# Performance work log

Measured on AMD Instinct MI355X. Metric: run time of the kernel, lower is better.

The kernel has to match this reference:

```python
import jax, jax.numpy as jnp
import numpy as np

HEADS = 16
DIM_HEAD = 64
SCALE = DIM_HEAD ** -0.5


def setup_inputs() -> dict:
    key = jax.random.key(0)
    k1, k2, k3 = jax.random.split(key, 3)
    dim, inner = 1024, HEADS * DIM_HEAD
    b, n = 2, 2048
    x = jax.random.normal(k1, (b, n, dim), dtype=jnp.float32)
    w_qkv = jax.random.normal(k2, (dim, 3 * inner), dtype=jnp.float32) * (dim ** -0.5)
    w_out = jax.random.normal(k3, (inner, dim), dtype=jnp.float32) * (inner ** -0.5)
    b_out = jnp.zeros((dim,), dtype=jnp.float32)
    return {"x": x, "w_qkv": w_qkv, "w_out": w_out, "b_out": b_out}


def reference(x, w_qkv, w_out, b_out):
    b, n, _ = x.shape
    qkv = x @ w_qkv                                   # [b,n,3*inner]
    q, k, v = jnp.split(qkv, 3, axis=-1)
    def to_heads(t):
        return t.reshape(b, n, HEADS, DIM_HEAD).transpose(0, 2, 1, 3)  # [b,h,n,d]
    q, k, v = to_heads(q), to_heads(k), to_heads(v)
    dots = jnp.einsum('bhid,bhjd->bhij', q, k) * SCALE  # [b,h,n,n]
    attn = jax.nn.softmax(dots, axis=-1)
    out = jnp.einsum('bhij,bhjd->bhid', attn, v)        # [b,h,n,d]
    out = out.transpose(0, 2, 1, 3).reshape(b, n, HEADS * DIM_HEAD)
    return out @ w_out + b_out
```

## Files before the change

### kernel.cpp

```cpp
#include <hip/hip_runtime.h>
#include <hip/hip_bf16.h>

typedef unsigned short u16;
typedef unsigned int u32;
typedef __attribute__((ext_vector_type(8))) short short8;
typedef __attribute__((ext_vector_type(4))) float f32x4;
typedef __attribute__((ext_vector_type(16))) float f32x16;
typedef __attribute__((ext_vector_type(2))) u32 u32x2;

typedef __attribute__((address_space(1))) void as1_void;
typedef __attribute__((address_space(3))) void as3_void;

__device__ __forceinline__ u16 f2b(float x) {
    union { float f; u32 u; } c; c.f = x;
    u32 r = c.u + 0x7fffu + ((c.u >> 16) & 1u);
    return (u16)(r >> 16);
}
__device__ __forceinline__ float b2f(u16 x) {
    union { u32 u; float f; } c; c.u = ((u32)x) << 16;
    return c.f;
}
__device__ __forceinline__ u32 cvtpk(float lo, float hi) {
    u32 r;
    asm("v_cvt_pk_bf16_f32 %0, %1, %2" : "=v"(r) : "v"(lo), "v"(hi));
    return r;
}
__device__ __forceinline__ void gload16(const u16* g, u16* l) {
    __builtin_amdgcn_global_load_lds((as1_void*)(u16*)g, (as3_void*)l, 16, 0, 0);
}
__device__ __forceinline__ void barrier_raw() {
    asm volatile("" ::: "memory");
    __builtin_amdgcn_s_barrier();
    asm volatile("" ::: "memory");
}

__device__ __forceinline__ void tbody(const float* __restrict__ in, u16* __restrict__ out,
                                      int R, int C, int r0, int c0, int t,
                                      u16 (&tile)[64][72]) {
    {
        const int rr = t >> 2;
        const int cq = (t & 3) * 16;
        const float* src = in + (size_t)(r0 + rr) * C + c0 + cq;
        #pragma unroll
        for (int j = 0; j < 4; j++) {
            float4 v = *(const float4*)(src + j * 4);
            tile[cq + j*4 + 0][rr] = f2b(v.x);
            tile[cq + j*4 + 1][rr] = f2b(v.y);
            tile[cq + j*4 + 2][rr] = f2b(v.z);
            tile[cq + j*4 + 3][rr] = f2b(v.w);
        }
    }
    __syncthreads();
    {
        const int cc = t >> 2;
        const int rq = (t & 3) * 16;
        u16* dst = out + (size_t)(c0 + cc) * R + r0 + rq;
        *(short8*)(dst)     = *(const short8*)&tile[cc][rq];
        *(short8*)(dst + 8) = *(const short8*)&tile[cc][rq + 8];
    }
}

__global__ __launch_bounds__(256) void prep_fused(const float* __restrict__ x,
                                                  const float* __restrict__ w_qkv,
                                                  const float* __restrict__ w_out,
                                                  u16* __restrict__ xb,
                                                  u16* __restrict__ wqkvT,
                                                  u16* __restrict__ woutT) {
    __shared__ u16 tile[64][72];
    const int b = blockIdx.x, t = threadIdx.x;
    if (b < 2048) {
        const int i = b * 256 + t;
        const float4* p = (const float4*)(x + (size_t)i * 8);
        float4 a = p[0], c = p[1];
        short8 v;
        v[0]=(short)f2b(a.x); v[1]=(short)f2b(a.y); v[2]=(short)f2b(a.z); v[3]=(short)f2b(a.w);
        v[4]=(short)f2b(c.x); v[5]=(short)f2b(c.y); v[6]=(short)f2b(c.z); v[7]=(short)f2b(c.w);
        *(short8*)(xb + (size_t)i * 8) = v;
    } else if (b < 2816) {
        const int bb = b - 2048;
        tbody(w_qkv, wqkvT, 1024, 3072, (bb / 48) * 64, (bb % 48) * 64, t, tile);
    } else {
        const int bb = b - 2816;
        tbody(w_out, woutT, 1024, 1024, (bb >> 4) * 64, (bb & 15) * 64, t, tile);
    }
}

__global__ __launch_bounds__(256) void gemm128(const u16* __restrict__ A,
                                               const u16* __restrict__ Bt,
                                               u16* __restrict__ Cp,
                                               u16* __restrict__ vt,
                                               int M, int Nn, int K) {
    __shared__ __align__(16) u16 a_lds[2][128 * 32];
    __shared__ __align__(16) u16 b_lds[2][128 * 32];
    const int tid = threadIdx.x;
    const int w = tid >> 6, l = tid & 63;
    const int l16 = l & 15, lg = l >> 4;
    const int nbx = gridDim.x;
    const int flat = blockIdx.x + nbx * blockIdx.y;
    const int cpx = (nbx * gridDim.y) >> 3;
    const int logical = (flat & 7) * cpx + (flat >> 3);
    const int m0 = (logical / nbx) * 128, n0 = (logical % nbx) * 128;
    const int wm = w >> 1, wn = w & 1;
    const int lr = l >> 2;
    const int scol = (((l & 3) ^ ((lr >> 1) & 3)) * 8);
    const int rsl = (lg ^ ((l16 >> 1) & 3)) * 8;

    f32x4 acc[4][4];
    #pragma unroll
    for (int i = 0; i < 4; i++)
        #pragma unroll
        for (int j = 0; j < 4; j++) { f32x4 z = {0.f,0.f,0.f,0.f}; acc[i][j] = z; }

    const u16* Ap = A  + (size_t)m0 * K;
    const u16* Bp = Bt + (size_t)n0 * K;

#define STAGE(BUF, KOF)                                                              \
    _Pragma("unroll")                                                                \
    for (int j = 0; j < 2; j++) {                                                    \
        const int r = w * 32 + j * 16;                                               \
        gload16(Ap + (size_t)(r + lr) * K + (KOF) + scol, &a_lds[(BUF)][r * 32]);    \
        gload16(Bp + (size_t)(r + lr) * K + (KOF) + scol, &b_lds[(BUF)][r * 32]);    \
    }

    const int nk = K >> 5;
    STAGE(0, 0)
    int cur = 0;
    for (int kt = 0; kt < nk; kt++) {
        if (kt + 1 < nk) {
            STAGE(cur ^ 1, (kt + 1) << 5)
            __builtin_amdgcn_sched_barrier(0);
            asm volatile("s_waitcnt vmcnt(4)" ::: "memory");
            __builtin_amdgcn_sched_barrier(0);
        } else {
            __builtin_amdgcn_sched_barrier(0);
            asm volatile("s_waitcnt vmcnt(0)" ::: "memory");
            __builtin_amdgcn_sched_barrier(0);
        }
        barrier_raw();
        short8 af[4], bf8[4];
        #pragma unroll
        for (int mb = 0; mb < 4; mb++)
            af[mb] = *(const short8*)&a_lds[cur][(wm * 64 + mb * 16 + l16) * 32 + rsl];
        #pragma unroll
        for (int nb = 0; nb < 4; nb++)
            bf8[nb] = *(const short8*)&b_lds[cur][(wn * 64 + nb * 16 + l16) * 32 + rsl];
        #pragma unroll
        for (int mb = 0; mb < 4; mb++)
            #pragma unroll
            for (int nb = 0; nb < 4; nb++)
                acc[mb][nb] = __builtin_amdgcn_mfma_f32_16x16x32_bf16(af[mb], bf8[nb], acc[mb][nb], 0, 0, 0);
        barrier_raw();
        cur ^= 1;
    }
#undef STAGE

    #pragma unroll
    for (int mb = 0; mb < 4; mb++) {
        #pragma unroll
        for (int nb = 0; nb < 4; nb++) {
            const int col = n0 + wn * 64 + nb * 16 + l16;
            const int row0 = m0 + wm * 64 + mb * 16 + lg * 4;
            if (col < 2048) {
                #pragma unroll
                for (int r = 0; r < 4; r++)
                    Cp[(size_t)(row0 + r) * Nn + col] = f2b(acc[mb][nb][r]);
            } else {
                const int hd = col - 2048;
                const int hh = hd >> 6, d = hd & 63;
                const int bi = row0 >> 11, n = row0 & 2047;
                u32x2 pr;
                pr.x = cvtpk(acc[mb][nb][0], acc[mb][nb][1]);
                pr.y = cvtpk(acc[mb][nb][2], acc[mb][nb][3]);
                *(u32x2*)(vt + ((size_t)((bi * 16 + hh) * 64 + d)) * 2048 + n) = pr;
            }
        }
    }
}

__global__ __launch_bounds__(256) void gemm64n(const u16* __restrict__ A,
                                               const u16* __restrict__ Bt,
                                               float* __restrict__ Cp,
                                               const float* __restrict__ bias,
                                               int M, int Nn, int K) {
    __shared__ __align__(16) u16 a_lds[2][64 * 32];
    __shared__ __align__(16) u16 b_lds[2][128 * 32];
    const int tid = threadIdx.x;
    const int w = tid >> 6, l = tid & 63;
    const int l16 = l & 15, lg = l >> 4;
    const int nbx = gridDim.x;
    const int flat = blockIdx.x + nbx * blockIdx.y;
    const int cpx = (nbx * gridDim.y) >> 3;
    const int logical = (flat & 7) * cpx + (flat >> 3);
    const int m0 = (logical / nbx) * 64, n0 = (logical % nbx) * 128;
    const int wm = w >> 1, wn = w & 1;
    const int lr = l >> 2;
    const int scol = (((l & 3) ^ ((lr >> 1) & 3)) * 8);
    const int rsl = (lg ^ ((l16 >> 1) & 3)) * 8;

    f32x4 acc[2][4];
    #pragma unroll
    for (int i = 0; i < 2; i++)
        #pragma unroll
        for (int j = 0; j < 4; j++) { f32x4 z = {0.f,0.f,0.f,0.f}; acc[i][j] = z; }

    const u16* Ap = A  + (size_t)m0 * K;
    const u16* Bp = Bt + (size_t)n0 * K;

#define STAGE64(BUF, KOF)                                                            \
    gload16(Ap + (size_t)(w * 16 + lr) * K + (KOF) + scol, &a_lds[(BUF)][w * 16 * 32]); \
    _Pragma("unroll")                                                                \
    for (int j = 0; j < 2; j++) {                                                    \
        const int r = w * 32 + j * 16;                                               \
        gload16(Bp + (size_t)(r + lr) * K + (KOF) + scol, &b_lds[(BUF)][r * 32]);    \
    }

    const int nk = K >> 5;
    STAGE64(0, 0)
    int cur = 0;
    for (int kt = 0; kt < nk; kt++) {
        if (kt + 1 < nk) {
            STAGE64(cur ^ 1, (kt + 1) << 5)
            __builtin_amdgcn_sched_barrier(0);
            asm volatile("s_waitcnt vmcnt(3)" ::: "memory");
            __builtin_amdgcn_sched_barrier(0);
        } else {
            __builtin_amdgcn_sched_barrier(0);
            asm volatile("s_waitcnt vmcnt(0)" ::: "memory");
            __builtin_amdgcn_sched_barrier(0);
        }
        barrier_raw();
        short8 af[2], bf8[4];
        #pragma unroll
        for (int mb = 0; mb < 2; mb++)
            af[mb] = *(const short8*)&a_lds[cur][(wm * 32 + mb * 16 + l16) * 32 + rsl];
        #pragma unroll
        for (int nb = 0; nb < 4; nb++)
            bf8[nb] = *(const short8*)&b_lds[cur][(wn * 64 + nb * 16 + l16) * 32 + rsl];
        #pragma unroll
        for (int mb = 0; mb < 2; mb++)
            #pragma unroll
            for (int nb = 0; nb < 4; nb++)
                acc[mb][nb] = __builtin_amdgcn_mfma_f32_16x16x32_bf16(af[mb], bf8[nb], acc[mb][nb], 0, 0, 0);
        barrier_raw();
        cur ^= 1;
    }
#undef STAGE64

    #pragma unroll
    for (int mb = 0; mb < 2; mb++) {
        #pragma unroll
        for (int nb = 0; nb < 4; nb++) {
            const int col = n0 + wn * 64 + nb * 16 + l16;
            const int row0 = m0 + wm * 32 + mb * 16 + lg * 4;
            #pragma unroll
            for (int r = 0; r < 4; r++)
                Cp[(size_t)(row0 + r) * Nn + col] = acc[mb][nb][r] + bias[col];
        }
    }
}

__global__ __launch_bounds__(256, 2) void attn_kernel(const u16* __restrict__ qkv,
                                                      const u16* __restrict__ vt,
                                                      u16* __restrict__ out) {
    __shared__ __align__(16) u16 k_lds[16384];
    __shared__ __align__(16) u16 v_lds[16384];
    const int tid = threadIdx.x;
    const int w = tid >> 6, l = tid & 63;
    const int l31 = l & 31, hi = l >> 5;
    const int flat = blockIdx.x + (blockIdx.y << 4) + (blockIdx.z << 8);
    const int logical = (flat & 7) * 64 + (flat >> 3);
    const int xq = logical & 15, h = (logical >> 4) & 15, bb = logical >> 8;
    const int q0 = xq * 128 + w * 32;
    const int swzl = (l31 & 7) << 3;

    const u16* qp = qkv + (size_t)(bb * 2048 + q0 + l31) * 3072 + h * 64 + hi * 8;
    short8 qf[4];
    #pragma unroll
    for (int c4 = 0; c4 < 4; c4++) {
        short8 v = *(const short8*)(qp + c4 * 16);
        #pragma unroll
        for (int e = 0; e < 8; e++) v[e] = (short)f2b(b2f((u16)v[e]) * 0.125f);
        qf[c4] = v;
    }

    f32x16 o[2];
    #pragma unroll
    for (int d0 = 0; d0 < 2; d0++)
        #pragma unroll
        for (int e = 0; e < 16; e++) o[d0][e] = 0.f;
    float mrow = -1e30f, lsum = 0.f;

    const int srow = tid >> 2, sc = tid & 3;
    const int kd0 = srow * 64 + ((sc ^ (srow & 7)) * 8);
    const int kd1 = srow * 64 + (((sc + 4) ^ (srow & 7)) * 8);
    const u16* ksrc = qkv + (size_t)(bb * 2048 + srow) * 3072 + 1024 + h * 64 + sc * 8;
    const u16* vsrc = vt + (size_t)((bb * 16 + h) * 64 + srow) * 2048 + sc * 8;

    short8 kr0, kr1, vr0, vr1;
    kr0 = *(const short8*)ksrc; kr1 = *(const short8*)(ksrc + 32);
    vr0 = *(const short8*)vsrc; vr1 = *(const short8*)(vsrc + 32);
    ksrc += 64 * 3072; vsrc += 64;
    *(short8*)&k_lds[kd0] = kr0; *(short8*)&k_lds[kd1] = kr1;
    *(short8*)&v_lds[kd0] = vr0; *(short8*)&v_lds[kd1] = vr1;
    kr0 = *(const short8*)ksrc; kr1 = *(const short8*)(ksrc + 32);
    vr0 = *(const short8*)vsrc; vr1 = *(const short8*)(vsrc + 32);
    ksrc += 64 * 3072; vsrc += 64;
    *(short8*)&k_lds[4096 + kd0] = kr0; *(short8*)&k_lds[4096 + kd1] = kr1;
    *(short8*)&v_lds[4096 + kd0] = vr0; *(short8*)&v_lds[4096 + kd1] = vr1;
    __syncthreads();

#define DO_TILE(CUR, NXT)                                                               \
  {                                                                                     \
    kr0 = *(const short8*)ksrc; kr1 = *(const short8*)(ksrc + 32);                      \
    vr0 = *(const short8*)vsrc; vr1 = *(const short8*)(vsrc + 32);                      \
    ksrc += 64 * 3072; vsrc += 64;                                                      \
    f32x16 st[2];                                                                       \
    _Pragma("unroll") for (int tt = 0; tt < 2; tt++)                                    \
      _Pragma("unroll") for (int e = 0; e < 16; e++) st[tt][e] = 0.f;                   \
    _Pragma("unroll")                                                                   \
    for (int c4 = 0; c4 < 4; c4++) {                                                    \
      short8 kf0 = *(const short8*)&k_lds[(CUR) + (l31)*64      + ((c4*16 + hi*8) ^ swzl)]; \
      short8 kf1 = *(const short8*)&k_lds[(CUR) + (32 + l31)*64 + ((c4*16 + hi*8) ^ swzl)]; \
      st[0] = __builtin_amdgcn_mfma_f32_32x32x16_bf16(kf0, qf[c4], st[0], 0, 0, 0);     \
      st[1] = __builtin_amdgcn_mfma_f32_32x32x16_bf16(kf1, qf[c4], st[1], 0, 0, 0);     \
    }                                                                                   \
    float pmax = st[0][0];                                                              \
    _Pragma("unroll") for (int e = 1; e < 16; e++) pmax = fmaxf(pmax, st[0][e]);        \
    _Pragma("unroll") for (int e = 0; e < 16; e++) pmax = fmaxf(pmax, st[1][e]);        \
    const float rowm = fmaxf(pmax, __shfl_xor(pmax, 32));                               \
    if (__any(rowm > mrow + 5.5451774f)) {              \
      const float mnew  = fmaxf(mrow, rowm);                                            \
      const float alpha = __expf(mrow - mnew);                                          \
      lsum *= alpha;                                                                    \
      _Pragma("unroll") for (int d0 = 0; d0 < 2; d0++)                                  \
        _Pragma("unroll") for (int e = 0; e < 16; e++) o[d0][e] *= alpha;               \
      mrow = mnew;                                                                      \
    }                                                                                   \
    _Pragma("unroll") for (int tt = 0; tt < 2; tt++)                                    \
      _Pragma("unroll") for (int e = 0; e < 16; e++) st[tt][e] = __expf(st[tt][e] - mrow); \
    float psum = 0.f;                                                                   \
    _Pragma("unroll") for (int tt = 0; tt < 2; tt++)                                    \
      _Pragma("unroll") for (int e = 0; e < 16; e++) psum += st[tt][e];                 \
    lsum += psum + __shfl_xor(psum, 32);                                                \
    short8 pb[4];                                                                       \
    _Pragma("unroll")                                                                   \
    for (int tt = 0; tt < 2; tt++) {                                                    \
      _Pragma("unroll")                                                                 \
      for (int g = 0; g < 2; g++) {                                                     \
         \
        u32 w0 = cvtpk(st[tt][8*g + 0], st[tt][8*g + 1]);                               \
        u32 w1 = cvtpk(st[tt][8*g + 2], st[tt][8*g + 3]);                               \
        u32 w2 = cvtpk(st[tt][8*g + 4], st[tt][8*g + 5]);                               \
        u32 w3 = cvtpk(st[tt][8*g + 6], st[tt][8*g + 7]);                               \
        u32 w0x = (u32)__shfl_xor((int)w0, 32);                                         \
        u32 w1x = (u32)__shfl_xor((int)w1, 32);                                         \
        u32 w2x = (u32)__shfl_xor((int)w2, 32);                                         \
        u32 w3x = (u32)__shfl_xor((int)w3, 32);                                         \
        union { u32 wd[4]; short8 s8; } uu;                                             \
        uu.wd[0] = hi ? w2x : w0;                                                       \
        uu.wd[1] = hi ? w3x : w1;                                                       \
        uu.wd[2] = hi ? w2  : w0x;                                                      \
        uu.wd[3] = hi ? w3  : w1x;                                                      \
        pb[2*tt + g] = uu.s8;                                                           \
      }                                                                                 \
    }                                                                                   \
    _Pragma("unroll")                                                                   \
    for (int ks = 0; ks < 4; ks++) {                                                    \
      short8 vf0 = *(const short8*)&v_lds[(CUR) + (l31)*64      + ((ks*16 + hi*8) ^ swzl)]; \
      short8 vf1 = *(const short8*)&v_lds[(CUR) + (32 + l31)*64 + ((ks*16 + hi*8) ^ swzl)]; \
      o[0] = __builtin_amdgcn_mfma_f32_32x32x16_bf16(vf0, pb[ks], o[0], 0, 0, 0);       \
      o[1] = __builtin_amdgcn_mfma_f32_32x32x16_bf16(vf1, pb[ks], o[1], 0, 0, 0);       \
    }                                                                                   \
    *(short8*)&k_lds[(NXT) + kd0] = kr0; *(short8*)&k_lds[(NXT) + kd1] = kr1;           \
    *(short8*)&v_lds[(NXT) + kd0] = vr0; *(short8*)&v_lds[(NXT) + kd1] = vr1;           \
  }

    for (int it = 0; it < 8; it++) {
        DO_TILE(0, 8192)
        DO_TILE(4096, 12288)
        __syncthreads();
        DO_TILE(8192, 0)
        DO_TILE(12288, 4096)
        __syncthreads();
    }
#undef DO_TILE

    const float invl = 1.0f / lsum;
    u16* op = out + (size_t)(bb * 2048 + q0 + l31) * 1024 + h * 64;
    #pragma unroll
    for (int d0 = 0; d0 < 2; d0++) {
        #pragma unroll
        for (int s = 0; s < 4; s++) {
            u32x2 pr;
            pr.x = cvtpk(o[d0][4*s + 0] * invl, o[d0][4*s + 1] * invl);
            pr.y = cvtpk(o[d0][4*s + 2] * invl, o[d0][4*s + 3] * invl);
            *(u32x2*)(op + d0 * 32 + s * 8 + hi * 4) = pr;
        }
    }
}

extern "C" void kernel_launch(void* const* d_in, const int* in_sizes, int n_in,
                              void* d_out, int out_size, void* d_ws, size_t ws_size,
                              hipStream_t stream) {
    const float* x     = (const float*)d_in[0];
    const float* w_qkv = (const float*)d_in[1];
    const float* w_out = (const float*)d_in[2];
    const float* b_out = (const float*)d_in[3];

    char* ws = (char*)d_ws;
    u16* xb    = (u16*)(ws);
    u16* wqkvT = (u16*)(ws + (size_t)( 8u << 20));
    u16* woutT = (u16*)(ws + (size_t)(14u << 20));
    u16* qkvb  = (u16*)(ws + (size_t)(16u << 20));
    u16* vtb   = (u16*)(ws + (size_t)(40u << 20));
    u16* aout  = (u16*)(ws + (size_t)(48u << 20));

    prep_fused<<<3072, 256, 0, stream>>>(x, w_qkv, w_out, xb, wqkvT, woutT);

    gemm128<<<dim3(24, 32), 256, 0, stream>>>(xb, wqkvT, qkvb, vtb, 4096, 3072, 1024);
    attn_kernel<<<dim3(16, 16, 2), 256, 0, stream>>>(qkvb, vtb, aout);

    gemm64n<<<dim3(8, 64), 256, 0, stream>>>(aout, woutT, (float*)d_out, b_out,
                                             4096, 1024, 1024);
}
```

Baseline: 118.5 us.

## Stage attention K/V tiles directly into LDS using pre-swizzled global layouts

The QKV GEMM epilogue now writes K and the transposed V in an XOR-swizzled order inside each 64-element block. The attention kernel can then copy tiles straight from global memory into LDS with gload16, instead of loading into registers and storing with a swizzle. This is meant to cut VGPR pressure and VALU/LDS-store instructions in the main loop and to let loads for the next pair of tiles run while the current pair is computed. The prefetch in the last loop iteration fetches tiles past the sequence end, which may read out of bounds unless the load is bounds-checked.

```diff
diff --git a/kernel.cpp b/kernel.cpp
--- a/kernel.cpp
+++ b/kernel.cpp
@@ -160,18 +160,28 @@
         for (int nb = 0; nb < 4; nb++) {
             const int col = n0 + wn * 64 + nb * 16 + l16;
             const int row0 = m0 + wm * 64 + mb * 16 + lg * 4;
-            if (col < 2048) {
+            if (col < 1024) {
                 #pragma unroll
                 for (int r = 0; r < 4; r++)
                     Cp[(size_t)(row0 + r) * Nn + col] = f2b(acc[mb][nb][r]);
+            } else if (col < 2048) {
+                const int d = col & 63;
+                const int cb = col & ~63;
+                #pragma unroll
+                for (int r = 0; r < 4; r++) {
+                    const int row = row0 + r;
+                    const int sw = (((d >> 3) ^ (row & 7)) << 3) | (d & 7);
+                    Cp[(size_t)row * Nn + cb + sw] = f2b(acc[mb][nb][r]);
+                }
             } else {
                 const int hd = col - 2048;
                 const int hh = hd >> 6, d = hd & 63;
                 const int bi = row0 >> 11, n = row0 & 2047;
+                const int n2 = (n & ~63) | (((((n >> 3) & 7) ^ (d & 7)) << 3)) | (n & 7);
                 u32x2 pr;
                 pr.x = cvtpk(acc[mb][nb][0], acc[mb][nb][1]);
                 pr.y = cvtpk(acc[mb][nb][2], acc[mb][nb][3]);
-                *(u32x2*)(vt + ((size_t)((bi * 16 + hh) * 64 + d)) * 2048 + n) = pr;
+                *(u32x2*)(vt + ((size_t)((bi * 16 + hh) * 64 + d)) * 2048 + n2) = pr;
             }
         }
     }
@@ -290,30 +300,26 @@
         for (int e = 0; e < 16; e++) o[d0][e] = 0.f;
     float mrow = -1e30f, lsum = 0.f;
 
-    const int srow = tid >> 2, sc = tid & 3;
-    const int kd0 = srow * 64 + ((sc ^ (srow & 7)) * 8);
-    const int kd1 = srow * 64 + (((sc + 4) ^ (srow & 7)) * 8);
-    const u16* ksrc = qkv + (size_t)(bb * 2048 + srow) * 3072 + 1024 + h * 64 + sc * 8;
-    const u16* vsrc = vt + (size_t)((bb * 16 + h) * 64 + srow) * 2048 + sc * 8;
-
-    short8 kr0, kr1, vr0, vr1;
-    kr0 = *(const short8*)ksrc; kr1 = *(const short8*)(ksrc + 32);
-    vr0 = *(const short8*)vsrc; vr1 = *(const short8*)(vsrc + 32);
-    ksrc += 64 * 3072; vsrc += 64;
-    *(short8*)&k_lds[kd0] = kr0; *(short8*)&k_lds[kd1] = kr1;
-    *(short8*)&v_lds[kd0] = vr0; *(short8*)&v_lds[kd1] = vr1;
-    kr0 = *(const short8*)ksrc; kr1 = *(const short8*)(ksrc + 32);
-    vr0 = *(const short8*)vsrc; vr1 = *(const short8*)(vsrc + 32);
-    ksrc += 64 * 3072; vsrc += 64;
-    *(short8*)&k_lds[4096 + kd0] = kr0; *(short8*)&k_lds[4096 + kd1] = kr1;
-    *(short8*)&v_lds[4096 + kd0] = vr0; *(short8*)&v_lds[4096 + kd1] = vr1;
+    const int wc0 = w * 2, wc1 = w * 2 + 1;
+    const int lrow = l >> 3, lsl = (l & 7) * 8;
+    const u16* kbase = qkv + (size_t)(bb * 2048) * 3072 + 1024 + h * 64 + lsl;
+    const u16* vbase = vt + (size_t)((bb * 16 + h) * 64) * 2048 + lsl;
+
+#define STAGE_ATTN(BUF, T)                                                              \
+  {                                                                                     \
+    const int j = (T) * 64;                                                             \
+    gload16(kbase + (size_t)(j + wc0 * 8 + lrow) * 3072, &k_lds[(BUF) + wc0 * 512]);    \
+    gload16(kbase + (size_t)(j + wc1 * 8 + lrow) * 3072, &k_lds[(BUF) + wc1 * 512]);    \
+    gload16(vbase + (size_t)(wc0 * 8 + lrow) * 2048 + j, &v_lds[(BUF) + wc0 * 512]);    \
+    gload16(vbase + (size_t)(wc1 * 8 + lrow) * 2048 + j, &v_lds[(BUF) + wc1 * 512]);    \
+  }
+
+    STAGE_ATTN(0, 0)
+    STAGE_ATTN(4096, 1)
     __syncthreads();
 
-#define DO_TILE(CUR, NXT)                                                               \
+#define DO_TILE(CUR)                                                                    \
   {                                                                                     \
-    kr0 = *(const short8*)ksrc; kr1 = *(const short8*)(ksrc + 32);                      \
-    vr0 = *(const short8*)vsrc; vr1 = *(const short8*)(vsrc + 32);                      \
-    ksrc += 64 * 3072; vsrc += 64;                                                      \
     f32x16 st[2];                                                                       \
     _Pragma("unroll") for (int tt = 0; tt < 2; tt++)                                    \
       _Pragma("unroll") for (int e = 0; e < 16; e++) st[tt][e] = 0.f;                   \
@@ -371,19 +377,23 @@
       o[0] = __builtin_amdgcn_mfma_f32_32x32x16_bf16(vf0, pb[ks], o[0], 0, 0, 0);       \
       o[1] = __builtin_amdgcn_mfma_f32_32x32x16_bf16(vf1, pb[ks], o[1], 0, 0, 0);       \
     }                                                                                   \
-    *(short8*)&k_lds[(NXT) + kd0] = kr0; *(short8*)&k_lds[(NXT) + kd1] = kr1;           \
-    *(short8*)&v_lds[(NXT) + kd0] = vr0; *(short8*)&v_lds[(NXT) + kd1] = vr1;           \
   }
 
     for (int it = 0; it < 8; it++) {
-        DO_TILE(0, 8192)
-        DO_TILE(4096, 12288)
+        const int t = it * 4;
+        STAGE_ATTN(8192, t + 2)
+        STAGE_ATTN(12288, t + 3)
+        DO_TILE(0)
+        DO_TILE(4096)
         __syncthreads();
-        DO_TILE(8192, 0)
-        DO_TILE(12288, 4096)
+        STAGE_ATTN(0, t + 4)
+        STAGE_ATTN(4096, t + 5)
+        DO_TILE(8192)
+        DO_TILE(12288)
         __syncthreads();
     }
 #undef DO_TILE
+#undef STAGE_ATTN
 
     const float invl = 1.0f / lsum;
     u16* op = out + (size_t)(bb * 2048 + q0 + l31) * 1024 + h * 64;
```

New measurement: 119.3 us. No clear change (+0.7%).
